# Performance work log

Measured on AMD Instinct MI355X. Metric: run time of the kernel, lower is better.

Reference implementation:

```python
import jax, jax.numpy as jnp
import numpy as np

EPS_FEAT = 1.0 + 1e-4   # feature_map offset: elu(x) + 1.0 + 0.0001
EPS_DEN = 1e-6


def setup_inputs() -> dict:
    key = jax.random.key(0)
    k1, k2, k3 = jax.random.split(key, 3)
    B, L, D = 4, 4096, 1024
    x = jax.random.normal(k1, (B, L, D), dtype=jnp.float32)
    # torch Linear-style init scale ~ 1/sqrt(fan_in)
    W_qkv = jax.random.normal(k2, (D, 3 * D), dtype=jnp.float32) / np.sqrt(D)
    b_qkv = jnp.zeros((3 * D,), dtype=jnp.float32)
    W_out = jax.random.normal(k3, (D, D), dtype=jnp.float32) / np.sqrt(D)
    b_out = jnp.zeros((D,), dtype=jnp.float32)
    return {"x": x, "W_qkv": W_qkv, "b_qkv": b_qkv, "W_out": W_out, "b_out": b_out}


def _linear_attention(x, W_qkv, b_qkv, W_out, b_out, num_heads=16):
    B, L, D = x.shape
    H = num_heads
    E = D // H

    qkv = x @ W_qkv + b_qkv                       # (B, L, 3D)
    q, k, v = jnp.split(qkv, 3, axis=-1)
    q = q.reshape(B, L, H, E)
    k = k.reshape(B, L, H, E)
    v = v.reshape(B, L, H, E)

    q = jax.nn.elu(q * (E ** -0.5)) + EPS_FEAT    # scale BEFORE feature map (as in source)
    k = jax.nn.elu(k) + EPS_FEAT

    # Causal linear attention via recurrence over L; math identical to
    # cumsum of k \otimes v outer products, but never materializes (B,L,H,E,E).
    qL = jnp.moveaxis(q, 1, 0)                    # (L, B, H, E)
    kL = jnp.moveaxis(k, 1, 0)
    vL = jnp.moveaxis(v, 1, 0)

    kv0 = jnp.zeros((B, H, E, E), dtype=x.dtype)
    ks0 = jnp.zeros((B, H, E), dtype=x.dtype)

    def step(carry, qkv_t):
        kv_s, k_s = carry
        q_t, k_t, v_t = qkv_t                     # each (B, H, E)
        kv_s = kv_s + jnp.einsum('bhe,bhf->bhef', k_t, v_t)
        k_s = k_s + k_t
        num = jnp.einsum('bhe,bhef->bhf', q_t, kv_s)           # (B, H, E)
        den = jnp.einsum('bhe,bhe->bh', q_t, k_s)[..., None] + EPS_DEN
        return (kv_s, k_s), num / den

    _, out = jax.lax.scan(step, (kv0, ks0), (qL, kL, vL))       # out: (L, B, H, E)
    out = jnp.moveaxis(out, 0, 1).reshape(B, L, D)
    # dropout is identity in eval mode
    return out @ W_out + b_out


def reference(x, W_qkv, b_qkv, W_out, b_out):
    return _linear_attention(x, W_qkv, b_qkv, W_out, b_out)
```

## Files before the change

### kernel.cpp

```cpp
#include <hip/hip_runtime.h>
#include <hip/hip_bf16.h>
#include <stdint.h>

#define B_ 4
#define L_ 4096
#define D_ 1024
#define H_ 16
#define E_ 64
#define M_ (B_*L_)
#define N1_ (3*D_)
#define CHK 128
#define NC (L_/CHK)
#define BH (B_*H_)

#define EPS_FEAT 1.0001f
#define EPS_DEN 1e-6f

typedef __attribute__((ext_vector_type(4))) float f32x4;
typedef __attribute__((ext_vector_type(8))) short bf16x8;

__device__ __forceinline__ unsigned short f2bf(float x) {
    union { float f; unsigned int u; } v; v.f = x;
    unsigned int r = v.u + 0x7FFFu + ((v.u >> 16) & 1u);
    return (unsigned short)(r >> 16);
}

__device__ __forceinline__ void gload_lds16(const unsigned short* g, unsigned short* l) {
    __builtin_amdgcn_global_load_lds(
        (const __attribute__((address_space(1))) unsigned int*)(const void*)g,
        (__attribute__((address_space(3))) unsigned int*)(void*)l,
        16, 0, 0);
}


__global__ __launch_bounds__(256) void cvt_x(const float* __restrict__ x,
                                             unsigned short* __restrict__ xb) {
    int i4 = blockIdx.x * 256 + threadIdx.x;
    float4 v = ((const float4*)x)[i4];
    unsigned int lo = (unsigned int)f2bf(v.x) | ((unsigned int)f2bf(v.y) << 16);
    unsigned int hi = (unsigned int)f2bf(v.z) | ((unsigned int)f2bf(v.w) << 16);
    ((uint2*)xb)[i4] = make_uint2(lo, hi);
}

__global__ __launch_bounds__(256) void transp_w(const float* __restrict__ W,
                                                unsigned short* __restrict__ WT,
                                                int K, int N) {
    __shared__ float tile[32][33];
    int kb = blockIdx.y * 32, nb = blockIdx.x * 32;
    int tx = threadIdx.x & 31, ty = threadIdx.x >> 5;
#pragma unroll
    for (int j = 0; j < 4; ++j)
        tile[ty + 8*j][tx] = W[(size_t)(kb + ty + 8*j) * N + nb + tx];
    __syncthreads();
#pragma unroll
    for (int j = 0; j < 4; ++j) {
        int nl = ty + 8*j;
        WT[(size_t)(nb + nl) * K + kb + tx] = f2bf(tile[tx][nl]);
    }
}


template<int MODE, int KDIM, int NDIM>
__global__ __launch_bounds__(512, 2) void gemm256(
    const unsigned short* __restrict__ A,
    const unsigned short* __restrict__ BT,
    const float* __restrict__ bias,
    float* __restrict__ outF,
    unsigned short* __restrict__ qf,
    unsigned short* __restrict__ kf,
    unsigned short* __restrict__ vf)
{
    __shared__ __align__(16) unsigned short smem[65536];

    const int t = threadIdx.x, lane = t & 63, w = t >> 6;
    const int wr = w >> 2, wc = w & 3;

    const int nwgx = NDIM / 256;
    const int nwg = nwgx * (M_ / 256);
    const int bid0 = blockIdx.y * nwgx + blockIdx.x;
    const int swz = (bid0 & 7) * (nwg >> 3) + (bid0 >> 3);
    const int m0 = (swz / nwgx) * 256, n0 = (swz % nwgx) * 256;
    const int lr = lane & 15, lg = lane >> 4;

    auto stage = [&](int T, int ab, int h) {
        unsigned short* base = smem + (T & 1) * 32768 + ab * 16384 + h * 8192;
        const unsigned short* src = ab ? BT : A;
        const int boff = (ab ? n0 : m0) + h * 128;
        const int kt = T * 64;
#pragma unroll
        for (int i = 0; i < 2; ++i) {
            int c = i * 512 + t;
            int rowl = c >> 3, s = c & 7;
            int col = ((s ^ (rowl & 7)) << 3);
            gload_lds16(src + (size_t)(boff + rowl) * KDIM + kt + col, &base[c * 8]);
        }
    };

    bf16x8 af[4][2], bq[4][2];
    f32x4 acc[8][4] = {};

    auto rdA = [&](const unsigned short* Ab, int m, int ks) {
        int row = wr * 128 + m * 16 + lr;
        int slot = (ks * 4 + lg) ^ (row & 7);
        return *(const bf16x8*)&Ab[row * 64 + slot * 8];
    };
    auto rdB = [&](const unsigned short* Bb, int n, int ks) {
        int row = wc * 64 + n * 16 + lr;
        int slot = (ks * 4 + lg) ^ (row & 7);
        return *(const bf16x8*)&Bb[row * 64 + slot * 8];
    };

#define PHASE_SYNC() \
    __builtin_amdgcn_s_barrier(); \
    asm volatile("s_waitcnt lgkmcnt(0)" ::: "memory"); \
    __builtin_amdgcn_sched_barrier(0); \
    __builtin_amdgcn_s_setprio(1);
#define PHASE_END() \
    __builtin_amdgcn_s_setprio(0); \
    __builtin_amdgcn_s_barrier();

    auto tile = [&](int T, bool s1, bool s2) {
        const unsigned short* Ab = smem + (T & 1) * 32768;
        const unsigned short* Bb = Ab + 16384;
#pragma unroll
        for (int m = 0; m < 4; ++m) { af[m][0] = rdA(Ab, m, 0); af[m][1] = rdA(Ab, m, 1); }
#pragma unroll
        for (int j = 0; j < 2; ++j) { bq[j][0] = rdB(Bb, j, 0); bq[j][1] = rdB(Bb, j, 1); }
        if (s1) stage(T + 1, 0, 0);
        PHASE_SYNC();
#pragma unroll
        for (int m = 0; m < 4; ++m)
#pragma unroll
            for (int j = 0; j < 2; ++j) {
                acc[m][j] = __builtin_amdgcn_mfma_f32_16x16x32_bf16(af[m][0], bq[j][0], acc[m][j], 0, 0, 0);
                acc[m][j] = __builtin_amdgcn_mfma_f32_16x16x32_bf16(af[m][1], bq[j][1], acc[m][j], 0, 0, 0);
            }
        PHASE_END();
#pragma unroll
        for (int j = 0; j < 2; ++j) { bq[2+j][0] = rdB(Bb, 2+j, 0); bq[2+j][1] = rdB(Bb, 2+j, 1); }
        if (s1) stage(T + 1, 0, 1);
        PHASE_SYNC();
#pragma unroll
        for (int m = 0; m < 4; ++m)
#pragma unroll
            for (int j = 0; j < 2; ++j) {
                acc[m][2+j] = __builtin_amdgcn_mfma_f32_16x16x32_bf16(af[m][0], bq[2+j][0], acc[m][2+j], 0, 0, 0);
                acc[m][2+j] = __builtin_amdgcn_mfma_f32_16x16x32_bf16(af[m][1], bq[2+j][1], acc[m][2+j], 0, 0, 0);
            }
        PHASE_END();
#pragma unroll
        for (int m = 0; m < 4; ++m) { af[m][0] = rdA(Ab, 4+m, 0); af[m][1] = rdA(Ab, 4+m, 1); }
        if (s2) stage(T + 2, 1, 0);
        PHASE_SYNC();
#pragma unroll
        for (int m = 0; m < 4; ++m)
#pragma unroll
            for (int j = 0; j < 2; ++j) {
                acc[4+m][j] = __builtin_amdgcn_mfma_f32_16x16x32_bf16(af[m][0], bq[j][0], acc[4+m][j], 0, 0, 0);
                acc[4+m][j] = __builtin_amdgcn_mfma_f32_16x16x32_bf16(af[m][1], bq[j][1], acc[4+m][j], 0, 0, 0);
            }
        PHASE_END();
        if (s2) stage(T + 2, 1, 1);
        PHASE_SYNC();
#pragma unroll
        for (int m = 0; m < 4; ++m)
#pragma unroll
            for (int j = 0; j < 2; ++j) {
                acc[4+m][2+j] = __builtin_amdgcn_mfma_f32_16x16x32_bf16(af[m][0], bq[2+j][0], acc[4+m][2+j], 0, 0, 0);
                acc[4+m][2+j] = __builtin_amdgcn_mfma_f32_16x16x32_bf16(af[m][1], bq[2+j][1], acc[4+m][2+j], 0, 0, 0);
            }
        __builtin_amdgcn_s_setprio(0);
    };

    constexpr int NT = KDIM / 64;
    stage(0, 0, 0); stage(0, 0, 1); stage(0, 1, 0); stage(0, 1, 1);
    stage(1, 1, 0); stage(1, 1, 1);
    asm volatile("s_waitcnt vmcnt(4)" ::: "memory");
    __builtin_amdgcn_s_barrier();
    __builtin_amdgcn_sched_barrier(0);

    for (int T = 0; T < NT - 2; ++T) {
        tile(T, true, T + 2 < NT);
        asm volatile("s_waitcnt vmcnt(4)" ::: "memory");
        __builtin_amdgcn_s_barrier();
        __builtin_amdgcn_sched_barrier(0);
    }
    tile(NT - 2, true, false);
    asm volatile("s_waitcnt vmcnt(0)" ::: "memory");
    __builtin_amdgcn_s_barrier();
    __builtin_amdgcn_sched_barrier(0);
    tile(NT - 1, false, false);
    __syncthreads();

    if (MODE == 0) {
        unsigned short* cbf = smem;
        const bool isQ = (n0 < D_), isK = (n0 >= D_ && n0 < 2*D_);
        const float scale = isQ ? 0.125f : 1.0f;
        unsigned short* buf = isQ ? qf : (isK ? kf : vf);
        const int b = m0 >> 12, l0 = m0 & 4095;
        const int h0 = (n0 & 1023) >> 6;
#pragma unroll
        for (int p = 0; p < 2; ++p) {
            if (wr == p) {
#pragma unroll
                for (int n = 0; n < 4; ++n) {
                    int cl = wc*64 + n*16 + lr;
                    float bv = bias[n0 + cl];
#pragma unroll
                    for (int m = 0; m < 8; ++m)
#pragma unroll
                        for (int q = 0; q < 4; ++q) {
                            int rl = m*16 + lg*4 + q;
                            float val = (acc[m][n][q] + bv) * scale;
                            float fv = (isQ || isK)
                                       ? ((val > 0.f ? val : __expf(val) - 1.f) + EPS_FEAT)
                                       : val;
                            cbf[rl * 264 + cl] = f2bf(fv);
                        }
                }
            }
            __syncthreads();
#pragma unroll
            for (int hh = 0; hh < 4; ++hh) {
                unsigned short* dst = buf + (((size_t)(b * H_ + h0 + hh)) * L_ + l0 + p*128) * E_;
#pragma unroll
                for (int i = 0; i < 2; ++i) {
                    int c = i*512 + t, row = c >> 3, ch = c & 7;
                    uint4 v = *(const uint4*)&cbf[row * 264 + hh*64 + ch*8];
                    *(uint4*)&dst[row * 64 + ch*8] = v;
                }
            }
            __syncthreads();
        }
    } else {
        float* cfl = (float*)smem;
#pragma unroll
        for (int p = 0; p < 4; ++p) {
            if (wr == (p >> 1)) {
                int mbase = (p & 1) * 4;
#pragma unroll
                for (int n = 0; n < 4; ++n) {
                    int cl = wc*64 + n*16 + lr;
                    float bv = bias[n0 + cl];
#pragma unroll
                    for (int mm = 0; mm < 4; ++mm)
#pragma unroll
                        for (int q = 0; q < 4; ++q) {
                            int rl = mm*16 + lg*4 + q;
                            cfl[rl * 260 + cl] = acc[mbase + mm][n][q] + bv;
                        }
                }
            }
            __syncthreads();
#pragma unroll
            for (int i = 0; i < 8; ++i) {
                int c = i*512 + t, row = c >> 6, ch = c & 63;
                float4 v = *(const float4*)&cfl[row * 260 + ch*4];
                *(float4*)&outF[(size_t)(m0 + p*64 + row) * NDIM + n0 + ch*4] = v;
            }
            __syncthreads();
        }
    }
#undef PHASE_SYNC
#undef PHASE_END
}


__global__ __launch_bounds__(256) void chunk_kv(
    const unsigned short* __restrict__ kf, const unsigned short* __restrict__ vf,
    float* __restrict__ kvout, float* __restrict__ ksout)
{
    constexpr int LDK = 136;
    __shared__ unsigned short Kt[64 * LDK];
    __shared__ unsigned short Vt[80 * LDK];

    int t = threadIdx.x, lane = t & 63, w = t >> 6;
    int bid = blockIdx.x;
    const unsigned short* kp = kf + (size_t)bid * CHK * E_;
    const unsigned short* vp = vf + (size_t)bid * CHK * E_;

#pragma unroll
    for (int it = 0; it < 4; ++it) {
        int s = it * 256 + t;
        int rl = s >> 3, e0 = (s & 7) << 3;
        uint4 kv8 = *(const uint4*)(kp + s * 8);
        uint4 vv8 = *(const uint4*)(vp + s * 8);
        unsigned int kw[4] = {kv8.x, kv8.y, kv8.z, kv8.w};
        unsigned int vw[4] = {vv8.x, vv8.y, vv8.z, vv8.w};
#pragma unroll
        for (int jw = 0; jw < 4; ++jw) {
            Kt[(e0 + 2*jw    ) * LDK + rl] = (unsigned short)(kw[jw] & 0xFFFF);
            Kt[(e0 + 2*jw + 1) * LDK + rl] = (unsigned short)(kw[jw] >> 16);
            Vt[(e0 + 2*jw    ) * LDK + rl] = (unsigned short)(vw[jw] & 0xFFFF);
            Vt[(e0 + 2*jw + 1) * LDK + rl] = (unsigned short)(vw[jw] >> 16);
        }
    }
    if (t < 128) Vt[64 * LDK + t] = 0x3F80;
    for (int i = t; i < 15 * LDK; i += 256) Vt[65 * LDK + i] = 0;
    __syncthreads();

    int lr = lane & 15, lg = lane >> 4;
    f32x4 acc[4] = {};
    f32x4 accE[4] = {};
#pragma unroll
    for (int ks = 0; ks < 4; ++ks) {
        bf16x8 a = *(const bf16x8*)&Vt[(w*16 + lr) * LDK + ks*32 + lg*8];
#pragma unroll
        for (int n = 0; n < 4; ++n) {
            bf16x8 b = *(const bf16x8*)&Kt[(n*16 + lr) * LDK + ks*32 + lg*8];
            acc[n] = __builtin_amdgcn_mfma_f32_16x16x32_bf16(a, b, acc[n], 0, 0, 0);
        }
    }
    if (w == 0) {
#pragma unroll
        for (int ks = 0; ks < 4; ++ks) {
            bf16x8 a = *(const bf16x8*)&Vt[(64 + lr) * LDK + ks*32 + lg*8];
#pragma unroll
            for (int n = 0; n < 4; ++n) {
                bf16x8 b = *(const bf16x8*)&Kt[(n*16 + lr) * LDK + ks*32 + lg*8];
                accE[n] = __builtin_amdgcn_mfma_f32_16x16x32_bf16(a, b, accE[n], 0, 0, 0);
            }
        }
    }
    float* kvo = kvout + (size_t)bid * E_ * E_;
#pragma unroll
    for (int n = 0; n < 4; ++n)
#pragma unroll
        for (int q = 0; q < 4; ++q) {
            int f = w*16 + lg*4 + q, e = n*16 + lr;
            kvo[f * 64 + e] = acc[n][q];
        }
    if (w == 0 && lg == 0) {
#pragma unroll
        for (int n = 0; n < 4; ++n)
            ksout[(size_t)bid * 64 + n*16 + lr] = accE[n][0];
    }
}


__global__ __launch_bounds__(256) void prefix_kv(
    const float* __restrict__ kv, const float* __restrict__ ks,
    unsigned short* __restrict__ kvb, unsigned short* __restrict__ ksb)
{
    int bh = blockIdx.y, part = blockIdx.x, t = threadIdx.x;
    int idx = part * 256 + t;
    float st = 0.f;
    for (int c = 0; c < NC; ++c) {
        float tmp = kv[((size_t)bh * NC + c) * 4096 + idx];
        kvb[((size_t)bh * NC + c) * 4096 + idx] = f2bf(st);
        st += tmp;
    }
    if (part == 0 && t < 64) {
        float s0 = 0.f;
        for (int c = 0; c < NC; ++c) {
            float tmp = ks[((size_t)bh * NC + c) * 64 + t];
            ksb[((size_t)bh * NC + c) * 64 + t] = f2bf(s0);
            s0 += tmp;
        }
    }
}


__global__ __launch_bounds__(256, 2) void attn_out(
    const unsigned short* __restrict__ qf, const unsigned short* __restrict__ kf,
    const unsigned short* __restrict__ vf, const unsigned short* __restrict__ kvb,
    const unsigned short* __restrict__ ksb, unsigned short* __restrict__ attn)
{
    constexpr int LK = 72;
    constexpr int LV = 136;
    __shared__ unsigned short Ks[128 * LK];
    __shared__ unsigned short Vt[64 * LV];
    __shared__ unsigned short Ss[128 * LV];

    int t = threadIdx.x, lane = t & 63, w = t >> 6;
    int bid = blockIdx.x;
    int bh = bid >> 5, c = bid & 31;
    const unsigned short* qp = qf + (size_t)bid * CHK * E_;
    const unsigned short* kp = kf + (size_t)bid * CHK * E_;
    const unsigned short* vp = vf + (size_t)bid * CHK * E_;
    const unsigned short* kvp = kvb + (size_t)bid * 4096;

    int lr = lane & 15, lg = lane >> 4;

    bf16x8 aq[2][2];
#pragma unroll
    for (int m = 0; m < 2; ++m)
#pragma unroll
        for (int ks = 0; ks < 2; ++ks)
            aq[m][ks] = *(const bf16x8*)(qp + (w*32 + m*16 + lr) * 64 + ks*32 + lg*8);

#pragma unroll
    for (int it = 0; it < 4; ++it) {
        int s = it * 256 + t;
        int r = s >> 3, e0 = (s & 7) << 3;
        uint4 kv = *(const uint4*)(kp + s * 8);
        uint4 vv = *(const uint4*)(vp + s * 8);
        *(uint4*)&Ks[r * LK + e0] = kv;
        unsigned int vw[4] = {vv.x, vv.y, vv.z, vv.w};
#pragma unroll
        for (int jw = 0; jw < 4; ++jw) {
            Vt[(e0 + 2*jw    ) * LV + r] = (unsigned short)(vw[jw] & 0xFFFF);
            Vt[(e0 + 2*jw + 1) * LV + r] = (unsigned short)(vw[jw] >> 16);
        }
    }
    bf16x8 zfrag = {0,0,0,0,0,0,0,0};
    bf16x8 bone = zfrag, bks[2] = {zfrag, zfrag};
    if (lr == 0) {
#pragma unroll
        for (int j = 0; j < 8; ++j) bone[j] = (short)0x3F80;
        bks[0] = *(const bf16x8*)&ksb[(size_t)bid * 64 + lg*8];
        bks[1] = *(const bf16x8*)&ksb[(size_t)bid * 64 + 32 + lg*8];
    }
    __syncthreads();

#pragma unroll
    for (int m = 0; m < 2; ++m) {
        int rbase = w * 32 + m * 16;
        int jmax = 2 * w + m;
        for (int jb = 0; jb < 8; ++jb) {
            if (jb <= jmax) {
                f32x4 sacc = {};
                bf16x8 b0 = *(const bf16x8*)&Ks[(jb*16 + lr) * LK + lg*8];
                bf16x8 b1 = *(const bf16x8*)&Ks[(jb*16 + lr) * LK + 32 + lg*8];
                sacc = __builtin_amdgcn_mfma_f32_16x16x32_bf16(aq[m][0], b0, sacc, 0, 0, 0);
                sacc = __builtin_amdgcn_mfma_f32_16x16x32_bf16(aq[m][1], b1, sacc, 0, 0, 0);
#pragma unroll
                for (int q = 0; q < 4; ++q) {
                    int r = rbase + lg*4 + q;
                    int j = jb*16 + lr;
                    Ss[r * LV + j] = (j <= r) ? f2bf(sacc[q]) : (unsigned short)0;
                }
            } else {
#pragma unroll
                for (int q = 0; q < 4; ++q) {
                    int r = rbase + lg*4 + q;
                    Ss[r * LV + jb*16 + lr] = 0;
                }
            }
        }
    }

    f32x4 oacc[2][5] = {};
#pragma unroll
    for (int m = 0; m < 2; ++m) {
        int rbase = w * 32 + m * 16;
#pragma unroll
        for (int ks = 0; ks < 2; ++ks) {
            bf16x8 a = aq[m][ks];
#pragma unroll
            for (int n = 0; n < 4; ++n) {
                bf16x8 b = *(const bf16x8*)&kvp[(n*16 + lr) * 64 + ks*32 + lg*8];
                oacc[m][n] = __builtin_amdgcn_mfma_f32_16x16x32_bf16(a, b, oacc[m][n], 0, 0, 0);
            }
            oacc[m][4] = __builtin_amdgcn_mfma_f32_16x16x32_bf16(a, bks[ks], oacc[m][4], 0, 0, 0);
        }
        for (int ks = 0; ks <= w; ++ks) {
            bf16x8 a = *(const bf16x8*)&Ss[(rbase + lr) * LV + ks*32 + lg*8];
#pragma unroll
            for (int n = 0; n < 4; ++n) {
                bf16x8 b = *(const bf16x8*)&Vt[(n*16 + lr) * LV + ks*32 + lg*8];
                oacc[m][n] = __builtin_amdgcn_mfma_f32_16x16x32_bf16(a, b, oacc[m][n], 0, 0, 0);
            }
            oacc[m][4] = __builtin_amdgcn_mfma_f32_16x16x32_bf16(a, bone, oacc[m][4], 0, 0, 0);
        }
    }

    int b_idx = bh >> 4, h_idx = bh & 15;
#pragma unroll
    for (int m = 0; m < 2; ++m) {
        int rbase = w * 32 + m * 16;
        float den[4];
#pragma unroll
        for (int q = 0; q < 4; ++q)
            den[q] = __shfl(oacc[m][4][q], lane & 48, 64) + EPS_DEN;
#pragma unroll
        for (int n = 0; n < 4; ++n) {
#pragma unroll
            for (int q = 0; q < 4; ++q) {
                int r = rbase + lg*4 + q;
                int lpos = c * CHK + r;
                int col = n*16 + lr;
                size_t dst = ((size_t)b_idx * L_ + lpos) * D_ + h_idx * 64 + col;
                attn[dst] = f2bf(oacc[m][n][q] / den[q]);
            }
        }
    }
}


extern "C" void kernel_launch(void* const* d_in, const int* in_sizes, int n_in,
                              void* d_out, int out_size, void* d_ws, size_t ws_size,
                              hipStream_t stream)
{
    const float* x    = (const float*)d_in[0];
    const float* Wqkv = (const float*)d_in[1];
    const float* bqkv = (const float*)d_in[2];
    const float* Wout = (const float*)d_in[3];
    const float* bout = (const float*)d_in[4];
    float* out = (float*)d_out;

    char* ws = (char*)d_ws;
    size_t off = 0;
    auto alloc = [&](size_t bytes) { void* p = ws + off; off += (bytes + 255) & ~(size_t)255; return p; };
    unsigned short* xb  = (unsigned short*)alloc((size_t)M_ * D_ * 2);
    unsigned short* WqT = (unsigned short*)alloc((size_t)N1_ * D_ * 2);
    unsigned short* WoT = (unsigned short*)alloc((size_t)D_ * D_ * 2);
    unsigned short* qfb = (unsigned short*)alloc((size_t)M_ * D_ * 2);
    unsigned short* kfb = (unsigned short*)alloc((size_t)M_ * D_ * 2);
    unsigned short* vfb = (unsigned short*)alloc((size_t)M_ * D_ * 2);
    float* kvw = (float*)alloc((size_t)BH * NC * E_ * E_ * 4);
    float* ksw = (float*)alloc((size_t)BH * NC * E_ * 4);
    unsigned short* kvb = (unsigned short*)alloc((size_t)BH * NC * E_ * E_ * 2);
    unsigned short* ksb = (unsigned short*)alloc((size_t)BH * NC * E_ * 2);
    unsigned short* attn = xb;

    cvt_x<<<(M_ * D_ / 4) / 256, 256, 0, stream>>>(x, xb);
    transp_w<<<dim3(N1_ / 32, D_ / 32), 256, 0, stream>>>(Wqkv, WqT, D_, N1_);
    transp_w<<<dim3(D_ / 32, D_ / 32), 256, 0, stream>>>(Wout, WoT, D_, D_);

    gemm256<0, D_, N1_><<<dim3(N1_ / 256, M_ / 256), 512, 0, stream>>>(
        xb, WqT, bqkv, nullptr, qfb, kfb, vfb);

    chunk_kv<<<BH * NC, 256, 0, stream>>>(kfb, vfb, kvw, ksw);
    prefix_kv<<<dim3(16, BH), 256, 0, stream>>>(kvw, ksw, kvb, ksb);
    attn_out<<<BH * NC, 256, 0, stream>>>(qfb, kfb, vfb, kvb, ksb, attn);

    gemm256<1, D_, D_><<<dim3(D_ / 256, M_ / 256), 512, 0, stream>>>(
        attn, WoT, bout, out, nullptr, nullptr, nullptr);
}
```

Measured before the change: 249.2 us.

## Balance causal work in attn_out, trim GEMM barriers, merge weight transposes

In attn_out, each wave now handles row-block pair (w, 7-w) instead of two adjacent row blocks. This evens out the triangular intra-chunk causal work across waves. The GEMM main loop drops the barrier that ended each MFMA phase, and the two stage calls for tile T+2 now issue together before the last phase, cutting barrier stalls. The two weight-transpose launches are merged into one 3D-grid launch. Dropping barriers relies on the remaining pre-phase barriers to keep LDS buffer reuse safe, so this carries some race risk.

Result: faster. 242.1 us (-2.8%).

```diff
diff --git a/kernel.cpp b/kernel.cpp
--- a/kernel.cpp
+++ b/kernel.cpp
@@ -42,9 +42,15 @@
     ((uint2*)xb)[i4] = make_uint2(lo, hi);
 }
 
-__global__ __launch_bounds__(256) void transp_w(const float* __restrict__ W,
-                                                unsigned short* __restrict__ WT,
-                                                int K, int N) {
+__global__ __launch_bounds__(256) void transp_w2(const float* __restrict__ W0,
+                                                 const float* __restrict__ W1,
+                                                 unsigned short* __restrict__ T0,
+                                                 unsigned short* __restrict__ T1) {
+    int z = blockIdx.z;
+    if (z == 1 && blockIdx.x >= (D_ / 32)) return;
+    const float* W = z ? W1 : W0;
+    unsigned short* WT = z ? T1 : T0;
+    int N = z ? D_ : N1_;
     __shared__ float tile[32][33];
     int kb = blockIdx.y * 32, nb = blockIdx.x * 32;
     int tx = threadIdx.x & 31, ty = threadIdx.x >> 5;
@@ -55,7 +61,7 @@
 #pragma unroll
     for (int j = 0; j < 4; ++j) {
         int nl = ty + 8*j;
-        WT[(size_t)(nb + nl) * K + kb + tx] = f2bf(tile[tx][nl]);
+        WT[(size_t)(nb + nl) * D_ + kb + tx] = f2bf(tile[tx][nl]);
     }
 }
 
@@ -110,14 +116,13 @@
         return *(const bf16x8*)&Bb[row * 64 + slot * 8];
     };
 
-#define PHASE_SYNC() \
+#define PHASE_PRE() \
     __builtin_amdgcn_s_barrier(); \
     asm volatile("s_waitcnt lgkmcnt(0)" ::: "memory"); \
     __builtin_amdgcn_sched_barrier(0); \
     __builtin_amdgcn_s_setprio(1);
-#define PHASE_END() \
-    __builtin_amdgcn_s_setprio(0); \
-    __builtin_amdgcn_s_barrier();
+#define PHASE_POST() \
+    __builtin_amdgcn_s_setprio(0);
 
     auto tile = [&](int T, bool s1, bool s2) {
         const unsigned short* Ab = smem + (T & 1) * 32768;
@@ -127,7 +132,7 @@
 #pragma unroll
         for (int j = 0; j < 2; ++j) { bq[j][0] = rdB(Bb, j, 0); bq[j][1] = rdB(Bb, j, 1); }
         if (s1) stage(T + 1, 0, 0);
-        PHASE_SYNC();
+        PHASE_PRE();
 #pragma unroll
         for (int m = 0; m < 4; ++m)
 #pragma unroll
@@ -135,11 +140,11 @@
                 acc[m][j] = __builtin_amdgcn_mfma_f32_16x16x32_bf16(af[m][0], bq[j][0], acc[m][j], 0, 0, 0);
                 acc[m][j] = __builtin_amdgcn_mfma_f32_16x16x32_bf16(af[m][1], bq[j][1], acc[m][j], 0, 0, 0);
             }
-        PHASE_END();
+        PHASE_POST();
 #pragma unroll
         for (int j = 0; j < 2; ++j) { bq[2+j][0] = rdB(Bb, 2+j, 0); bq[2+j][1] = rdB(Bb, 2+j, 1); }
         if (s1) stage(T + 1, 0, 1);
-        PHASE_SYNC();
+        PHASE_PRE();
 #pragma unroll
         for (int m = 0; m < 4; ++m)
 #pragma unroll
@@ -147,11 +152,10 @@
                 acc[m][2+j] = __builtin_amdgcn_mfma_f32_16x16x32_bf16(af[m][0], bq[2+j][0], acc[m][2+j], 0, 0, 0);
                 acc[m][2+j] = __builtin_amdgcn_mfma_f32_16x16x32_bf16(af[m][1], bq[2+j][1], acc[m][2+j], 0, 0, 0);
             }
-        PHASE_END();
+        PHASE_POST();
 #pragma unroll
         for (int m = 0; m < 4; ++m) { af[m][0] = rdA(Ab, 4+m, 0); af[m][1] = rdA(Ab, 4+m, 1); }
-        if (s2) stage(T + 2, 1, 0);
-        PHASE_SYNC();
+        PHASE_PRE();
 #pragma unroll
         for (int m = 0; m < 4; ++m)
 #pragma unroll
@@ -159,9 +163,9 @@
                 acc[4+m][j] = __builtin_amdgcn_mfma_f32_16x16x32_bf16(af[m][0], bq[j][0], acc[4+m][j], 0, 0, 0);
                 acc[4+m][j] = __builtin_amdgcn_mfma_f32_16x16x32_bf16(af[m][1], bq[j][1], acc[4+m][j], 0, 0, 0);
             }
-        PHASE_END();
-        if (s2) stage(T + 2, 1, 1);
-        PHASE_SYNC();
+        PHASE_POST();
+        if (s2) { stage(T + 2, 1, 0); stage(T + 2, 1, 1); }
+        PHASE_PRE();
 #pragma unroll
         for (int m = 0; m < 4; ++m)
 #pragma unroll
@@ -169,7 +173,7 @@
                 acc[4+m][2+j] = __builtin_amdgcn_mfma_f32_16x16x32_bf16(af[m][0], bq[2+j][0], acc[4+m][2+j], 0, 0, 0);
                 acc[4+m][2+j] = __builtin_amdgcn_mfma_f32_16x16x32_bf16(af[m][1], bq[2+j][1], acc[4+m][2+j], 0, 0, 0);
             }
-        __builtin_amdgcn_s_setprio(0);
+        PHASE_POST();
     };
 
     constexpr int NT = KDIM / 64;
@@ -180,7 +184,7 @@
     __builtin_amdgcn_sched_barrier(0);
 
     for (int T = 0; T < NT - 2; ++T) {
-        tile(T, true, T + 2 < NT);
+        tile(T, true, true);
         asm volatile("s_waitcnt vmcnt(4)" ::: "memory");
         __builtin_amdgcn_s_barrier();
         __builtin_amdgcn_sched_barrier(0);
@@ -261,8 +265,8 @@
             __syncthreads();
         }
     }
-#undef PHASE_SYNC
-#undef PHASE_END
+#undef PHASE_PRE
+#undef PHASE_POST
 }
 
 
@@ -381,13 +385,14 @@
     const unsigned short* kvp = kvb + (size_t)bid * 4096;
 
     int lr = lane & 15, lg = lane >> 4;
+    const int jsel[2] = {w, 7 - w};
 
     bf16x8 aq[2][2];
 #pragma unroll
-    for (int m = 0; m < 2; ++m)
+    for (int mi = 0; mi < 2; ++mi)
 #pragma unroll
         for (int ks = 0; ks < 2; ++ks)
-            aq[m][ks] = *(const bf16x8*)(qp + (w*32 + m*16 + lr) * 64 + ks*32 + lg*8);
+            aq[mi][ks] = *(const bf16x8*)(qp + (jsel[mi]*16 + lr) * 64 + ks*32 + lg*8);
 
 #pragma unroll
     for (int it = 0; it < 4; ++it) {
@@ -414,21 +419,22 @@
     __syncthreads();
 
 #pragma unroll
-    for (int m = 0; m < 2; ++m) {
-        int rbase = w * 32 + m * 16;
-        int jmax = 2 * w + m;
-        for (int jb = 0; jb < 8; ++jb) {
-            if (jb <= jmax) {
+    for (int mi = 0; mi < 2; ++mi) {
+        int j = jsel[mi];
+        int rbase = j * 16;
+        int jbmax = j | 1;
+        for (int jb = 0; jb <= jbmax; ++jb) {
+            if (jb <= j) {
                 f32x4 sacc = {};
                 bf16x8 b0 = *(const bf16x8*)&Ks[(jb*16 + lr) * LK + lg*8];
                 bf16x8 b1 = *(const bf16x8*)&Ks[(jb*16 + lr) * LK + 32 + lg*8];
-                sacc = __builtin_amdgcn_mfma_f32_16x16x32_bf16(aq[m][0], b0, sacc, 0, 0, 0);
-                sacc = __builtin_amdgcn_mfma_f32_16x16x32_bf16(aq[m][1], b1, sacc, 0, 0, 0);
+                sacc = __builtin_amdgcn_mfma_f32_16x16x32_bf16(aq[mi][0], b0, sacc, 0, 0, 0);
+                sacc = __builtin_amdgcn_mfma_f32_16x16x32_bf16(aq[mi][1], b1, sacc, 0, 0, 0);
 #pragma unroll
                 for (int q = 0; q < 4; ++q) {
                     int r = rbase + lg*4 + q;
-                    int j = jb*16 + lr;
-                    Ss[r * LV + j] = (j <= r) ? f2bf(sacc[q]) : (unsigned short)0;
+                    int jj = jb*16 + lr;
+                    Ss[r * LV + jj] = (jj <= r) ? f2bf(sacc[q]) : (unsigned short)0;
                 }
             } else {
 #pragma unroll
@@ -442,37 +448,38 @@
 
     f32x4 oacc[2][5] = {};
 #pragma unroll
-    for (int m = 0; m < 2; ++m) {
-        int rbase = w * 32 + m * 16;
+    for (int mi = 0; mi < 2; ++mi) {
+        int j = jsel[mi];
+        int rbase = j * 16;
 #pragma unroll
         for (int ks = 0; ks < 2; ++ks) {
-            bf16x8 a = aq[m][ks];
+            bf16x8 a = aq[mi][ks];
 #pragma unroll
             for (int n = 0; n < 4; ++n) {
                 bf16x8 b = *(const bf16x8*)&kvp[(n*16 + lr) * 64 + ks*32 + lg*8];
-                oacc[m][n] = __builtin_amdgcn_mfma_f32_16x16x32_bf16(a, b, oacc[m][n], 0, 0, 0);
-            }
-            oacc[m][4] = __builtin_amdgcn_mfma_f32_16x16x32_bf16(a, bks[ks], oacc[m][4], 0, 0, 0);
-        }
-        for (int ks = 0; ks <= w; ++ks) {
+                oacc[mi][n] = __builtin_amdgcn_mfma_f32_16x16x32_bf16(a, b, oacc[mi][n], 0, 0, 0);
+            }
+            oacc[mi][4] = __builtin_amdgcn_mfma_f32_16x16x32_bf16(a, bks[ks], oacc[mi][4], 0, 0, 0);
+        }
+        for (int ks = 0; ks <= (j >> 1); ++ks) {
             bf16x8 a = *(const bf16x8*)&Ss[(rbase + lr) * LV + ks*32 + lg*8];
 #pragma unroll
             for (int n = 0; n < 4; ++n) {
                 bf16x8 b = *(const bf16x8*)&Vt[(n*16 + lr) * LV + ks*32 + lg*8];
-                oacc[m][n] = __builtin_amdgcn_mfma_f32_16x16x32_bf16(a, b, oacc[m][n], 0, 0, 0);
-            }
-            oacc[m][4] = __builtin_amdgcn_mfma_f32_16x16x32_bf16(a, bone, oacc[m][4], 0, 0, 0);
+                oacc[mi][n] = __builtin_amdgcn_mfma_f32_16x16x32_bf16(a, b, oacc[mi][n], 0, 0, 0);
+            }
+            oacc[mi][4] = __builtin_amdgcn_mfma_f32_16x16x32_bf16(a, bone, oacc[mi][4], 0, 0, 0);
         }
     }
 
     int b_idx = bh >> 4, h_idx = bh & 15;
 #pragma unroll
-    for (int m = 0; m < 2; ++m) {
-        int rbase = w * 32 + m * 16;
+    for (int mi = 0; mi < 2; ++mi) {
+        int rbase = jsel[mi] * 16;
         float den[4];
 #pragma unroll
         for (int q = 0; q < 4; ++q)
-            den[q] = __shfl(oacc[m][4][q], lane & 48, 64) + EPS_DEN;
+            den[q] = __shfl(oacc[mi][4][q], lane & 48, 64) + EPS_DEN;
 #pragma unroll
         for (int n = 0; n < 4; ++n) {
 #pragma unroll
@@ -481,7 +488,7 @@
                 int lpos = c * CHK + r;
                 int col = n*16 + lr;
                 size_t dst = ((size_t)b_idx * L_ + lpos) * D_ + h_idx * 64 + col;
-                attn[dst] = f2bf(oacc[m][n][q] / den[q]);
+                attn[dst] = f2bf(oacc[mi][n][q] / den[q]);
             }
         }
     }
@@ -515,8 +522,7 @@
     unsigned short* attn = xb;
 
     cvt_x<<<(M_ * D_ / 4) / 256, 256, 0, stream>>>(x, xb);
-    transp_w<<<dim3(N1_ / 32, D_ / 32), 256, 0, stream>>>(Wqkv, WqT, D_, N1_);
-    transp_w<<<dim3(D_ / 32, D_ / 32), 256, 0, stream>>>(Wout, WoT, D_, D_);
+    transp_w2<<<dim3(N1_ / 32, D_ / 32, 2), 256, 0, stream>>>(Wqkv, Wout, WqT, WoT);
 
     gemm256<0, D_, N1_><<<dim3(N1_ / 256, M_ / 256), 512, 0, stream>>>(
         xb, WqT, bqkv, nullptr, qfb, kfb, vfb);
```
